# Performance work log

Measured on AMD Instinct MI355X. Metric: run time of the kernel, lower is better.

## Reference

```python
import jax, jax.numpy as jnp
import numpy as np

_EPS = 1e-5

def _ln(x, g, b):
    m = jnp.mean(x, axis=-1, keepdims=True)
    v = jnp.var(x, axis=-1, keepdims=True)
    return (x - m) * jax.lax.rsqrt(v + _EPS) * g + b

def setup_inputs() -> dict:
    key = jax.random.key(0)
    ks = jax.random.split(key, 12)
    B, S, D = 8, 2048, 1024
    H = 2 * D          # hidden_dim = 2*n_embd
    A = H // 16        # adapt_dim = 128
    E = 8              # num_experts
    std = 1.0 / D ** 0.5
    astd = std * 0.01
    f = lambda k, shape, s: jax.random.normal(k, shape, dtype=jnp.float32) * s
    return {
        'x': f(ks[0], (B, S, D), 1.0),
        'expert_weights': f(ks[1], (B, S, E), 1.0),
        'w_up': f(ks[2], (H, D), std),
        'w_gate': f(ks[3], (H, D), std),
        'w_down': f(ks[4], (D, H), std),
        'w_pre': f(ks[5], (A, D), astd),
        'w_post': f(ks[6], (A, H), astd),
        'an_g': jnp.ones((A,), jnp.float32),
        'an_b': jnp.zeros((A,), jnp.float32),
        'w_aproj': f(ks[7], (H, A), astd),
        'w_exp': f(ks[8], (E, A, A), 0.01 / A ** 0.5),
        'eln_g': jnp.ones((E, A), jnp.float32),
        'eln_b': jnp.zeros((E, A), jnp.float32),
        'w_eproj': f(ks[9], (H, A), 0.01 / A ** 0.5),
        'w_out': f(ks[10], (D, H), 0.01 / A ** 0.5),
    }

def reference(x, expert_weights, w_up, w_gate, w_down, w_pre, w_post,
              an_g, an_b, w_aproj, w_exp, eln_g, eln_b, w_eproj, w_out):
    # ---- shared LLaDAExpert ----
    up = jnp.einsum('bsd,hd->bsh', x, w_up)
    gate = jnp.einsum('bsd,hd->bsh', x, w_gate)
    hidden = jax.nn.silu(gate) * up                      # [B,S,H]
    pre = jnp.einsum('bsd,ad->bsa', x, w_pre)            # pre_adapt(x), reused by experts
    adapt_in = _ln(pre, an_g, an_b)                      # [B,S,A]
    adapt_out = _ln(jnp.einsum('bsh,ah->bsa', hidden, w_post), an_g, an_b)
    aw = jax.nn.silu(jnp.clip(jnp.einsum('bsa,bta->bst', adapt_in, adapt_out), -5.0, 5.0))  # [B,S,S]
    adapt = jnp.einsum('bst,bta->bsa', aw, adapt_in)     # [B,S,A]
    hidden = hidden + 0.1 * jnp.einsum('bsa,ha->bsh', adapt, w_aproj)
    shared = jnp.einsum('bsh,dh->bsd', hidden, w_down)   # [B,S,D]
    combined = jnp.zeros_like(shared)
    E = w_exp.shape[0]
    for i in range(E):
        a = _ln(jnp.einsum('bsa,ca->bsc', pre, w_exp[i]), eln_g[i], eln_b[i])
        o = jnp.einsum('bsh,dh->bsd', jnp.einsum('bsc,hc->bsh', a, w_eproj), w_out)
        mask = expert_weights[:, :, i] > 0
        combined = jnp.where(mask[..., None], o, combined)
    return shared + 0.1 * combined
```

## Files before the change

### kernel.cpp

```cpp
#include <hip/hip_runtime.h>

#define TOK 16384
#define DD 1024
#define HH 2048
#define AA 128
#define EE 8
#define SS 2048
#define BB 8

typedef __attribute__((ext_vector_type(8))) short short8;
typedef __attribute__((ext_vector_type(4))) float floatx4;

__device__ __forceinline__ unsigned short f2b(float f) {
  unsigned u = __float_as_uint(f);
  u += 0x7fff + ((u >> 16) & 1);
  return (unsigned short)(u >> 16);
}
__device__ __forceinline__ float b2f(unsigned short h) {
  return __uint_as_float(((unsigned)h) << 16);
}

__device__ __forceinline__ void xcd_swizzle(int& bx, int& by) {
  const int nbx = gridDim.x, nby = gridDim.y;
  if ((nby & 7) == 0) {
    const int L = blockIdx.y * nbx + blockIdx.x;
    const int xcd = L & 7, idx = L >> 3;
    bx = idx % nbx;
    by = (xcd * (nby >> 3)) + idx / nbx;
  } else {
    bx = blockIdx.x; by = blockIdx.y;
  }
}


__device__ __forceinline__ void gload16(const short* g, short* l) {
  __builtin_amdgcn_global_load_lds((__attribute__((address_space(1))) void*)(void*)g,
                                   (__attribute__((address_space(3))) void*)l, 16, 0, 0);
}

__device__ __forceinline__ void stage_half(const short* src, int ld, short* dst, int wave, int h) {
  gload16(src + (long)(2*h)  *64*ld, dst + (2*h)  *4096 + wave*512);
  gload16(src + (long)(2*h+1)*64*ld, dst + (2*h+1)*4096 + wave*512);
}

#define MFMA_Q(M0, N0)                                                                   \
  __builtin_amdgcn_s_setprio(1);                                                         \
  _Pragma("unroll")                                                                      \
  for (int kk = 0; kk < 2; ++kk)                                                         \
    _Pragma("unroll")                                                                    \
    for (int m = 0; m < 4; ++m)                                                          \
      _Pragma("unroll")                                                                  \
      for (int n = 0; n < 2; ++n)                                                        \
        acc[M0+m][N0+n] = __builtin_amdgcn_mfma_f32_16x16x32_bf16(af[M0+m][kk], bf[N0+n][kk], acc[M0+m][N0+n], 0, 0, 0); \
  __builtin_amdgcn_s_setprio(0);

#define PHASE_END                                                                        \
  asm volatile("s_waitcnt lgkmcnt(0)" ::: "memory");                                     \
  __builtin_amdgcn_s_barrier();                                                          \
  asm volatile("" ::: "memory");

__device__ __forceinline__ void ktile8(const char* cA, const char* cB,
                                       short* nAd, short* cBd,
                                       const short* sA1, int lA1,
                                       const short* sB2, int lB2,
                                       bool stA, bool stB, int wave,
                                       int aOff, int bOff, int slot0, int slot1,
                                       floatx4 (*acc)[4])
{
  short8 af[8][2], bf[4][2];
#pragma unroll
  for (int m = 0; m < 4; ++m) {
    af[m][0] = *(const short8*)(cA + aOff + m*2048 + slot0);
    af[m][1] = *(const short8*)(cA + aOff + m*2048 + slot1);
  }
#pragma unroll
  for (int n = 0; n < 2; ++n) {
    bf[n][0] = *(const short8*)(cB + bOff + n*2048 + slot0);
    bf[n][1] = *(const short8*)(cB + bOff + n*2048 + slot1);
  }
  if (stA) stage_half(sA1, lA1, nAd, wave, 0);
  MFMA_Q(0, 0)
  PHASE_END
#pragma unroll
  for (int n = 2; n < 4; ++n) {
    bf[n][0] = *(const short8*)(cB + bOff + n*2048 + slot0);
    bf[n][1] = *(const short8*)(cB + bOff + n*2048 + slot1);
  }
  if (stA) stage_half(sA1, lA1, nAd, wave, 1);
  MFMA_Q(0, 2)
  PHASE_END
#pragma unroll
  for (int m = 4; m < 8; ++m) {
    af[m][0] = *(const short8*)(cA + aOff + m*2048 + slot0);
    af[m][1] = *(const short8*)(cA + aOff + m*2048 + slot1);
  }
  if (stB) stage_half(sB2, lB2, cBd, wave, 0);
  MFMA_Q(4, 0)
  PHASE_END
  if (stB) stage_half(sB2, lB2, cBd, wave, 1);
  MFMA_Q(4, 2)
  asm volatile("s_waitcnt lgkmcnt(0)" ::: "memory");
  if (stB) asm volatile("s_waitcnt vmcnt(4)" ::: "memory");
  else     asm volatile("s_waitcnt vmcnt(0)" ::: "memory");
  __builtin_amdgcn_s_barrier();
  asm volatile("" ::: "memory");
}

template<int EPI, bool SEG2>
__global__ __launch_bounds__(512, 2)
void gemm256(const unsigned short* __restrict__ Ag, int lda,
             const unsigned short* __restrict__ Bg, int ldb,
             void* __restrict__ Cg, int ldc,
             const unsigned short* __restrict__ Xg, int ldx,
             int K1,
             const unsigned short* __restrict__ A2g, int lda2,
             const unsigned short* __restrict__ B2g, int ldb2,
             int K2)
{
  __shared__ __align__(16) short As0[256*64], As1[256*64];
  __shared__ __align__(16) short Bs0[256*64], Bs1[256*64];
  int bx, by; xcd_swizzle(bx, by);
  const int tid = threadIdx.x;
  const int lane = tid & 63, wave = tid >> 6;
  const int q = lane >> 4, l15 = lane & 15;
  const int wm = wave >> 2, wn = wave & 3;

  const int arow = tid >> 3;
  const int kc8  = ((tid & 7) ^ (arow & 7)) * 8;

  const short* a1 = (const short*)Ag + (long)(by*256 + arow)*lda + kc8;
  const short* b1 = (const short*)Bg + (long)(bx*256 + arow)*ldb + kc8;
  const short* a2 = SEG2 ? (const short*)A2g + (long)(by*256 + arow)*lda2 + kc8 : (const short*)0;
  const short* b2 = SEG2 ? (const short*)B2g + (long)(bx*256 + arow)*ldb2 + kc8 : (const short*)0;
  const int nt1 = K1 >> 6, nt = SEG2 ? ((K1 + K2) >> 6) : (K1 >> 6);

  auto tA = [&](int T, const short*& p, int& ld) {
    if (!SEG2 || T < nt1) { p = a1 + T*64; ld = lda; } else { p = a2 + (T - nt1)*64; ld = lda2; }
  };
  auto tB = [&](int T, const short*& p, int& ld) {
    if (!SEG2 || T < nt1) { p = b1 + T*64; ld = ldb; } else { p = b2 + (T - nt1)*64; ld = ldb2; }
  };

  const int aOff  = (wm*128 + l15) * 128;
  const int bOff  = (wn*64  + l15) * 128;
  const int l7    = l15 & 7;
  const int slot0 = ((0*4 + q) ^ l7) * 16;
  const int slot1 = ((1*4 + q) ^ l7) * 16;

  floatx4 acc[8][4] = {};

  stage_half(a1, lda, As0, wave, 0); stage_half(a1, lda, As0, wave, 1);
  stage_half(b1, ldb, Bs0, wave, 0); stage_half(b1, ldb, Bs0, wave, 1);
  {
    const short *pb; int lb;
    tB(1, pb, lb);
    stage_half(pb, lb, Bs1, wave, 0); stage_half(pb, lb, Bs1, wave, 1);
  }
  asm volatile("s_waitcnt vmcnt(4)" ::: "memory");
  __builtin_amdgcn_s_barrier();
  asm volatile("" ::: "memory");

  for (int t = 0; t < nt; t += 2) {
    const short *sa, *sb; int la, lb;
    {
      const bool stA = (t+1) < nt, stB = (t+2) < nt;
      sa = a1; la = lda; sb = b1; lb = ldb;
      if (stA) tA(t+1, sa, la);
      if (stB) tB(t+2, sb, lb);
      ktile8((const char*)As0, (const char*)Bs0, As1, Bs0,
             sa, la, sb, lb, stA, stB, wave, aOff, bOff, slot0, slot1, acc);
    }
    {
      const bool stA = (t+2) < nt, stB = (t+3) < nt;
      sa = a1; la = lda; sb = b1; lb = ldb;
      if (stA) tA(t+2, sa, la);
      if (stB) tB(t+3, sb, lb);
      ktile8((const char*)As1, (const char*)Bs1, As0, Bs1,
             sa, la, sb, lb, stA, stB, wave, aOff, bOff, slot0, slot1, acc);
    }
  }

#pragma unroll
  for (int m = 0; m < 8; ++m)
#pragma unroll
    for (int n = 0; n < 4; ++n)
#pragma unroll
      for (int r = 0; r < 4; ++r) {
        const int row = by*256 + wm*128 + m*16 + q*4 + r;
        const int col = bx*256 + wn*64  + n*16 + l15;
        const long ci = (long)row*ldc + col;
        float v = acc[m][n][r];
        if (EPI == 0) {
          ((float*)Cg)[ci] = v;
        } else if (EPI == 1) {
          v = v / (1.f + __expf(-v));
          ((unsigned short*)Cg)[ci] = f2b(v);
        } else if (EPI == 2) {
          float g = b2f(Xg[(long)row*ldx + col]);
          ((unsigned short*)Cg)[ci] = f2b(v * g);
        }
      }
}

__device__ __forceinline__ void kloop_pipe(const short* Ap, int lda, const short* Bp, int ldb,
                                           short* As, short* Bs, int K,
                                           int tid, int q, int l15, int l7, int wm, int wn,
                                           floatx4 (*acc)[4])
{
  short8 pa[4], pb[4];
#pragma unroll
  for (int i = 0; i < 4; ++i) {
    pa[i] = *(const short8*)(Ap + (long)i*32*lda);
    pb[i] = *(const short8*)(Bp + (long)i*32*ldb);
  }
  for (int kt = 0; kt < K; kt += 64) {
#pragma unroll
    for (int i = 0; i < 4; ++i) {
      *(short8*)((char*)As + i*4096 + tid*16) = pa[i];
      *(short8*)((char*)Bs + i*4096 + tid*16) = pb[i];
    }
    __syncthreads();
    if (kt + 64 < K) {
#pragma unroll
      for (int i = 0; i < 4; ++i) {
        pa[i] = *(const short8*)(Ap + (long)i*32*lda + kt + 64);
        pb[i] = *(const short8*)(Bp + (long)i*32*ldb + kt + 64);
      }
    }
#pragma unroll
    for (int s = 0; s < 2; ++s) {
      short8 af[4], bf[4];
      const int slotoff = ((s*4 + q) ^ l7) * 16;
#pragma unroll
      for (int i = 0; i < 4; ++i) {
        af[i] = *(const short8*)((const char*)As + (wm*64 + i*16 + l15)*128 + slotoff);
        bf[i] = *(const short8*)((const char*)Bs + (wn*64 + i*16 + l15)*128 + slotoff);
      }
#pragma unroll
      for (int i = 0; i < 4; ++i)
#pragma unroll
        for (int j = 0; j < 4; ++j)
          acc[i][j] = __builtin_amdgcn_mfma_f32_16x16x32_bf16(af[i], bf[j], acc[i][j], 0, 0, 0);
    }
    __syncthreads();
  }
}

__global__ void cast_f32_bf16(const float* __restrict__ in, unsigned short* __restrict__ out, long n4) {
  long i = (long)blockIdx.x * blockDim.x + threadIdx.x;
  const long stride = (long)gridDim.x * blockDim.x;
  for (; i < n4; i += stride) {
    float4 v = ((const float4*)in)[i];
    ushort4 o;
    o.x = f2b(v.x); o.y = f2b(v.y); o.z = f2b(v.z); o.w = f2b(v.w);
    ((ushort4*)out)[i] = o;
  }
}

__global__ void transpose_cast(const float* __restrict__ in, unsigned short* __restrict__ out,
                               int R, int C) {
  __shared__ float t[32][33];
  const int lx = threadIdx.x & 31, ly = threadIdx.x >> 5;
  const int r0 = blockIdx.y * 32, c0 = blockIdx.x * 32;
#pragma unroll
  for (int i = 0; i < 32; i += 8)
    t[ly + i][lx] = in[(long)(r0 + ly + i) * C + (c0 + lx)];
  __syncthreads();
#pragma unroll
  for (int i = 0; i < 32; i += 8)
    out[(long)(c0 + ly + i) * R + (r0 + lx)] = f2b(t[lx][ly + i]);
}

template<int EPI>
__global__ __launch_bounds__(256)
void gemm_bt(const unsigned short* __restrict__ Ag, long sAz, int lda,
             const unsigned short* __restrict__ Bg, long sBz, int ldb,
             void* __restrict__ Cg, long sCz, int ldc,
             const unsigned short* __restrict__ Xg, long sXz, int ldx,
             int K)
{
  __shared__ __align__(16) short As[128*64];
  __shared__ __align__(16) short Bs[128*64];
  int bx, by; xcd_swizzle(bx, by);
  const int tid  = threadIdx.x;
  const int lane = tid & 63, wave = tid >> 6;
  const int q = lane >> 4, l15 = lane & 15, l7 = lane & 7;
  const int wm = wave & 1, wn = wave >> 1;

  const int arow = tid >> 3;
  const int kc8  = ((tid & 7) ^ (arow & 7)) * 8;

  const short* Ap = (const short*)Ag + (long)blockIdx.z*sAz + (long)(by*128 + arow)*lda + kc8;
  const short* Bp = (const short*)Bg + (long)blockIdx.z*sBz + (long)(bx*128 + arow)*ldb + kc8;

  floatx4 acc[4][4] = {};
  kloop_pipe(Ap, lda, Bp, ldb, As, Bs, K, tid, q, l15, l7, wm, wn, acc);

  const long cz = (long)blockIdx.z * sCz;
  const long xz = (long)blockIdx.z * sXz;
#pragma unroll
  for (int i = 0; i < 4; ++i)
#pragma unroll
    for (int j = 0; j < 4; ++j)
#pragma unroll
      for (int r = 0; r < 4; ++r) {
        const int row = by*128 + wm*64 + i*16 + q*4 + r;
        const int col = bx*128 + wn*64 + j*16 + l15;
        const long ci = cz + (long)row*ldc + col;
        float v = acc[i][j][r];
        if (EPI == 0) {
          ((float*)Cg)[ci] = v;
        } else if (EPI == 1) {
          v = v / (1.f + __expf(-v));
          ((unsigned short*)Cg)[ci] = f2b(v);
        } else if (EPI == 2) {
          float g = b2f(Xg[xz + (long)row*ldx + col]);
          ((unsigned short*)Cg)[ci] = f2b(v * g);
        } else if (EPI == 3) {
          ((unsigned short*)Cg)[ci] = f2b(v);
        } else if (EPI == 4) {
          v = fminf(fmaxf(v, -5.f), 5.f);
          v = v / (1.f + __expf(-v));
          ((unsigned short*)Cg)[ci] = f2b(v);
        } else if (EPI == 6) {
          ((unsigned short*)Cg)[ci] = f2b(0.1f * v);
        }
      }
}

__global__ void ln_rows(const float* __restrict__ X, const float* __restrict__ X2,
                        const float* __restrict__ g,
                        const float* __restrict__ b, unsigned short* __restrict__ lnout,
                        unsigned short* __restrict__ rawout, unsigned short* __restrict__ tout)
{
  const int lane = threadIdx.x & 63, wave = threadIdx.x >> 6;
  const long t = (long)blockIdx.x*4 + wave;
  const float* x  = X  + t*AA;
  const float* x2 = X2 + t*AA;
  float x0 = x[lane]      + x2[lane];
  float x1 = x[lane + 64] + x2[lane + 64];
  float s = x0 + x1, s2 = x0*x0 + x1*x1;
#pragma unroll
  for (int m = 1; m < 64; m <<= 1) {
    s  += __shfl_xor(s, m, 64);
    s2 += __shfl_xor(s2, m, 64);
  }
  float mean = s * (1.f/AA);
  float inv  = rsqrtf(s2*(1.f/AA) - mean*mean + 1e-5f);
  float y0 = (x0 - mean)*inv*g[lane] + b[lane];
  float y1 = (x1 - mean)*inv*g[lane+64] + b[lane+64];
  lnout[t*AA + lane]      = f2b(y0);
  lnout[t*AA + lane + 64] = f2b(y1);
  if (rawout) { rawout[t*AA+lane] = f2b(x0); rawout[t*AA+lane+64] = f2b(x1); }
  if (tout) {
    const long bb = t >> 11, si = t & (SS-1);
    tout[bb*(long)AA*SS + (long)lane*SS + si]      = f2b(y0);
    tout[bb*(long)AA*SS + (long)(lane+64)*SS + si] = f2b(y1);
  }
}

__global__ void expert_select_ln(const float* __restrict__ ew, const unsigned short* __restrict__ eall,
                                 const float* __restrict__ eg, const float* __restrict__ ebias,
                                 unsigned short* __restrict__ Fc)
{
  const int lane = threadIdx.x & 63, wave = threadIdx.x >> 6;
  const long t = (long)blockIdx.x*4 + wave;
  const float* w = ew + t*EE;
  int ie = -1;
#pragma unroll
  for (int i = 0; i < EE; ++i) if (w[i] > 0.f) ie = i;
  unsigned short o0 = 0, o1 = 0;
  if (ie >= 0) {
    float x0 = b2f(eall[t*(EE*AA) + ie*AA + lane]);
    float x1 = b2f(eall[t*(EE*AA) + ie*AA + lane + 64]);
    float s = x0 + x1, s2 = x0*x0 + x1*x1;
#pragma unroll
    for (int m = 1; m < 64; m <<= 1) { s += __shfl_xor(s, m, 64); s2 += __shfl_xor(s2, m, 64); }
    float mean = s * (1.f/AA);
    float inv  = rsqrtf(s2*(1.f/AA) - mean*mean + 1e-5f);
    o0 = f2b((x0-mean)*inv*eg[ie*AA+lane]    + ebias[ie*AA+lane]);
    o1 = f2b((x1-mean)*inv*eg[ie*AA+lane+64] + ebias[ie*AA+lane+64]);
  }
  Fc[t*256 + lane]      = o0;
  Fc[t*256 + lane + 64] = o1;
}

extern "C" void kernel_launch(void* const* d_in, const int* in_sizes, int n_in,
                              void* d_out, int out_size, void* d_ws, size_t ws_size,
                              hipStream_t stream)
{
  const float* x       = (const float*)d_in[0];
  const float* ew      = (const float*)d_in[1];
  const float* w_up    = (const float*)d_in[2];
  const float* w_gate  = (const float*)d_in[3];
  const float* w_down  = (const float*)d_in[4];
  const float* w_pre   = (const float*)d_in[5];
  const float* w_post  = (const float*)d_in[6];
  const float* an_g    = (const float*)d_in[7];
  const float* an_b    = (const float*)d_in[8];
  const float* w_aproj = (const float*)d_in[9];
  const float* w_exp   = (const float*)d_in[10];
  const float* eln_g   = (const float*)d_in[11];
  const float* eln_b   = (const float*)d_in[12];
  const float* w_eproj = (const float*)d_in[13];
  const float* w_out   = (const float*)d_in[14];

  char* ws = (char*)d_ws;
  size_t off = 0;
  auto take = [&](size_t bytes) { char* p = ws + off; off += (bytes + 255) & ~(size_t)255; return p; };

  unsigned short* Sc    = (unsigned short*)take((size_t)BB*SS*SS*2);
  unsigned short* xb    = Sc;
  unsigned short* eall  = (unsigned short*)((char*)Sc + (size_t)TOK*DD*2);
  unsigned short* hid   = (unsigned short*)take((size_t)TOK*HH*2);
  float*          pre   = (float*)take((size_t)TOK*AA*4*2);
  float*          postA = (float*)take((size_t)TOK*AA*4*2);
  unsigned short* Fc    = (unsigned short*)take((size_t)TOK*256*2);
  unsigned short* ain   = (unsigned short*)take((size_t)TOK*AA*2);
  unsigned short* ainT  = (unsigned short*)take((size_t)TOK*AA*2);
  unsigned short* aout  = (unsigned short*)take((size_t)TOK*AA*2);
  unsigned short* preb  = (unsigned short*)take((size_t)TOK*AA*2);
  unsigned short* wgb   = (unsigned short*)take((size_t)HH*DD*2);
  unsigned short* wub   = (unsigned short*)take((size_t)HH*DD*2);
  unsigned short* wdb   = (unsigned short*)take((size_t)DD*HH*2);
  unsigned short* wpostb= (unsigned short*)take((size_t)AA*HH*2);
  unsigned short* wpreb = (unsigned short*)take((size_t)AA*DD*2);
  unsigned short* wexpb = (unsigned short*)take((size_t)EE*AA*AA*2);
  unsigned short* Wc    = (unsigned short*)take((size_t)DD*256*2);
  (void)ws_size; (void)in_sizes; (void)n_in; (void)out_size;

  unsigned short* woutb  = hid;
  unsigned short* btT    = hid + (size_t)DD*HH;
  unsigned short* eprojT = btT;
  unsigned short* aprojT = btT + (size_t)AA*HH;

  cast_f32_bf16<<<1024, 256, 0, stream>>>(x,      xb,     (long)TOK*DD/4);
  cast_f32_bf16<<<256,  256, 0, stream>>>(w_gate, wgb,    (long)HH*DD/4);
  cast_f32_bf16<<<256,  256, 0, stream>>>(w_up,   wub,    (long)HH*DD/4);
  cast_f32_bf16<<<256,  256, 0, stream>>>(w_down, wdb,    (long)DD*HH/4);
  cast_f32_bf16<<<256,  256, 0, stream>>>(w_out,  woutb,  (long)DD*HH/4);
  cast_f32_bf16<<<64,   256, 0, stream>>>(w_post, wpostb, (long)AA*HH/4);
  cast_f32_bf16<<<32,   256, 0, stream>>>(w_pre,  wpreb,  (long)AA*DD/4);
  cast_f32_bf16<<<32,   256, 0, stream>>>(w_exp,  wexpb,  (long)EE*AA*AA/4);

  transpose_cast<<<dim3(AA/32, HH/32), 256, 0, stream>>>(w_eproj, eprojT, HH, AA);
  transpose_cast<<<dim3(AA/32, HH/32), 256, 0, stream>>>(w_aproj, aprojT, HH, AA);

  gemm_bt<6><<<dim3(1, DD/128, 2), 256, 0, stream>>>(
      woutb, (long)(wdb - woutb), HH,
      eprojT, (long)AA*HH, HH,
      Wc, AA, 256, nullptr, 0, 0, HH);

  gemm256<1, false><<<dim3(HH/256, TOK/256), 512, 0, stream>>>(
      xb, DD, wgb, DD, hid, HH, nullptr, 0, DD, nullptr, 0, nullptr, 0, 0);
  gemm256<2, false><<<dim3(HH/256, TOK/256), 512, 0, stream>>>(
      xb, DD, wub, DD, hid, HH, hid, HH, DD, nullptr, 0, nullptr, 0, 0);

  gemm_bt<0><<<dim3(1, TOK/128, 2), 256, 0, stream>>>(
      xb, DD/2, DD, wpreb, DD/2, DD, pre, (long)TOK*AA, AA, nullptr, 0, 0, DD/2);
  ln_rows<<<TOK/4, 256, 0, stream>>>(pre, pre + (size_t)TOK*AA, an_g, an_b, ain, preb, ainT);

  gemm_bt<3><<<dim3((EE*AA)/128, TOK/128, 1), 256, 0, stream>>>(preb,0,AA, wexpb,0,AA, eall,0,EE*AA, nullptr,0,0, AA);
  expert_select_ln<<<TOK/4, 256, 0, stream>>>(ew, eall, eln_g, eln_b, Fc);

  gemm_bt<0><<<dim3(1, TOK/128, 2), 256, 0, stream>>>(
      hid, HH/2, HH, wpostb, HH/2, HH, postA, (long)TOK*AA, AA, nullptr, 0, 0, HH/2);
  ln_rows<<<TOK/4, 256, 0, stream>>>(postA, postA + (size_t)TOK*AA, an_g, an_b, aout, nullptr, nullptr);

  gemm_bt<4><<<dim3(SS/128, SS/128, BB), 256, 0, stream>>>(ain,(long)SS*AA,AA, aout,(long)SS*AA,AA,
                                                           Sc,(long)SS*SS,SS, nullptr,0,0, AA);
  gemm_bt<3><<<dim3(1, SS/128, BB), 256, 0, stream>>>(Sc,(long)SS*SS,SS, ainT,(long)AA*SS,SS,
                                                      Fc+AA,(long)SS*256,256, nullptr,0,0, SS);
  gemm256<0, true><<<dim3(DD/256, TOK/256), 512, 0, stream>>>(
      hid, HH, wdb, HH, (float*)d_out, DD, nullptr, 0, HH, Fc, 256, Wc, 256, 256);
}
```

Measured before the change: 572.2 us.

## Rebalance gemm256 A/B staging, fuse weight casts, split-K the adapt GEMM

The 256x256 GEMM k-loop now prefetches A tiles further ahead, spreading the A and B half-tile global loads more evenly across the four MFMA phases and raising the allowed in-flight count. The eight separate f32-to-bf16 cast launches become one multi-job kernel to cut launch overhead. The aw·adapt_in GEMM, which had only 128 blocks, is split along K into two halves written to fp32 scratch, then summed and cast into Fc by a small extra kernel. This adds parallelism and removes launches in exchange for extra scratch traffic, an additional kernel, and a risk that pre-buffer reuse or the vmcnt accounting is wrong.

```diff
diff --git a/kernel.cpp b/kernel.cpp
--- a/kernel.cpp
+++ b/kernel.cpp
@@ -60,10 +60,11 @@
   asm volatile("" ::: "memory");
 
 __device__ __forceinline__ void ktile8(const char* cA, const char* cB,
-                                       short* nAd, short* cBd,
+                                       short* oAd, short* cAd, short* cBd,
                                        const short* sA1, int lA1,
+                                       const short* sA2, int lA2,
                                        const short* sB2, int lB2,
-                                       bool stA, bool stB, int wave,
+                                       bool st1, bool st2, int wave,
                                        int aOff, int bOff, int slot0, int slot1,
                                        floatx4 (*acc)[4])
 {
@@ -78,7 +79,7 @@
     bf[n][0] = *(const short8*)(cB + bOff + n*2048 + slot0);
     bf[n][1] = *(const short8*)(cB + bOff + n*2048 + slot1);
   }
-  if (stA) stage_half(sA1, lA1, nAd, wave, 0);
+  if (st1) stage_half(sA1, lA1, oAd, wave, 1);
   MFMA_Q(0, 0)
   PHASE_END
 #pragma unroll
@@ -86,7 +87,6 @@
     bf[n][0] = *(const short8*)(cB + bOff + n*2048 + slot0);
     bf[n][1] = *(const short8*)(cB + bOff + n*2048 + slot1);
   }
-  if (stA) stage_half(sA1, lA1, nAd, wave, 1);
   MFMA_Q(0, 2)
   PHASE_END
 #pragma unroll
@@ -94,13 +94,16 @@
     af[m][0] = *(const short8*)(cA + aOff + m*2048 + slot0);
     af[m][1] = *(const short8*)(cA + aOff + m*2048 + slot1);
   }
-  if (stB) stage_half(sB2, lB2, cBd, wave, 0);
+  if (st2) stage_half(sB2, lB2, cBd, wave, 0);
   MFMA_Q(4, 0)
   PHASE_END
-  if (stB) stage_half(sB2, lB2, cBd, wave, 1);
+  if (st2) {
+    stage_half(sB2, lB2, cBd, wave, 1);
+    stage_half(sA2, lA2, cAd, wave, 0);
+  }
   MFMA_Q(4, 2)
   asm volatile("s_waitcnt lgkmcnt(0)" ::: "memory");
-  if (stB) asm volatile("s_waitcnt vmcnt(4)" ::: "memory");
+  if (st2) asm volatile("s_waitcnt vmcnt(6)" ::: "memory");
   else     asm volatile("s_waitcnt vmcnt(0)" ::: "memory");
   __builtin_amdgcn_s_barrier();
   asm volatile("" ::: "memory");
@@ -152,31 +155,34 @@
   stage_half(a1, lda, As0, wave, 0); stage_half(a1, lda, As0, wave, 1);
   stage_half(b1, ldb, Bs0, wave, 0); stage_half(b1, ldb, Bs0, wave, 1);
   {
-    const short *pb; int lb;
-    tB(1, pb, lb);
+    const short *pb, *pa; int lb, la;
+    tB(1, pb, lb); tA(1, pa, la);
     stage_half(pb, lb, Bs1, wave, 0); stage_half(pb, lb, Bs1, wave, 1);
-  }
-  asm volatile("s_waitcnt vmcnt(4)" ::: "memory");
+    stage_half(pa, la, As1, wave, 0);
+  }
+  asm volatile("s_waitcnt vmcnt(6)" ::: "memory");
   __builtin_amdgcn_s_barrier();
   asm volatile("" ::: "memory");
 
   for (int t = 0; t < nt; t += 2) {
-    const short *sa, *sb; int la, lb;
+    const short *pa1, *pa2, *pb2; int la1, la2, lb2;
     {
-      const bool stA = (t+1) < nt, stB = (t+2) < nt;
-      sa = a1; la = lda; sb = b1; lb = ldb;
-      if (stA) tA(t+1, sa, la);
-      if (stB) tB(t+2, sb, lb);
-      ktile8((const char*)As0, (const char*)Bs0, As1, Bs0,
-             sa, la, sb, lb, stA, stB, wave, aOff, bOff, slot0, slot1, acc);
+      const bool st1 = (t+1) < nt, st2 = (t+2) < nt;
+      pa1 = a1; la1 = lda; pa2 = a1; la2 = lda; pb2 = b1; lb2 = ldb;
+      if (st1) tA(t+1, pa1, la1);
+      if (st2) { tA(t+2, pa2, la2); tB(t+2, pb2, lb2); }
+      ktile8((const char*)As0, (const char*)Bs0, As1, As0, Bs0,
+             pa1, la1, pa2, la2, pb2, lb2, st1, st2, wave,
+             aOff, bOff, slot0, slot1, acc);
     }
     {
-      const bool stA = (t+2) < nt, stB = (t+3) < nt;
-      sa = a1; la = lda; sb = b1; lb = ldb;
-      if (stA) tA(t+2, sa, la);
-      if (stB) tB(t+3, sb, lb);
-      ktile8((const char*)As1, (const char*)Bs1, As0, Bs1,
-             sa, la, sb, lb, stA, stB, wave, aOff, bOff, slot0, slot1, acc);
+      const bool st1 = (t+2) < nt, st2 = (t+3) < nt;
+      pa1 = a1; la1 = lda; pa2 = a1; la2 = lda; pb2 = b1; lb2 = ldb;
+      if (st1) tA(t+2, pa1, la1);
+      if (st2) { tA(t+3, pa2, la2); tB(t+3, pb2, lb2); }
+      ktile8((const char*)As1, (const char*)Bs1, As0, As1, Bs1,
+             pa1, la1, pa2, la2, pb2, lb2, st1, st2, wave,
+             aOff, bOff, slot0, slot1, acc);
     }
   }
 
@@ -246,14 +252,24 @@
   }
 }
 
-__global__ void cast_f32_bf16(const float* __restrict__ in, unsigned short* __restrict__ out, long n4) {
+struct CastJobs {
+  const float* src[8];
+  unsigned short* dst[8];
+  long end[8];
+};
+__global__ void cast_multi(CastJobs jobs, long total4) {
   long i = (long)blockIdx.x * blockDim.x + threadIdx.x;
   const long stride = (long)gridDim.x * blockDim.x;
-  for (; i < n4; i += stride) {
-    float4 v = ((const float4*)in)[i];
-    ushort4 o;
-    o.x = f2b(v.x); o.y = f2b(v.y); o.z = f2b(v.z); o.w = f2b(v.w);
-    ((ushort4*)out)[i] = o;
+  for (; i < total4; i += stride) {
+    int r = 0; long base = 0;
+#pragma unroll
+    for (int k = 0; k < 7; ++k)
+      if (i >= jobs.end[k]) { r = k + 1; base = jobs.end[k]; }
+    const long o = i - base;
+    float4 v = ((const float4*)jobs.src[r])[o];
+    ushort4 u;
+    u.x = f2b(v.x); u.y = f2b(v.y); u.z = f2b(v.z); u.w = f2b(v.w);
+    ((ushort4*)jobs.dst[r])[o] = u;
   }
 }
 
@@ -271,7 +287,7 @@
     out[(long)(c0 + ly + i) * R + (r0 + lx)] = f2b(t[lx][ly + i]);
 }
 
-template<int EPI>
+template<int EPI, bool SK2 = false>
 __global__ __launch_bounds__(256)
 void gemm_bt(const unsigned short* __restrict__ Ag, long sAz, int lda,
              const unsigned short* __restrict__ Bg, long sBz, int ldb,
@@ -290,14 +306,17 @@
   const int arow = tid >> 3;
   const int kc8  = ((tid & 7) ^ (arow & 7)) * 8;
 
-  const short* Ap = (const short*)Ag + (long)blockIdx.z*sAz + (long)(by*128 + arow)*lda + kc8;
-  const short* Bp = (const short*)Bg + (long)blockIdx.z*sBz + (long)(bx*128 + arow)*ldb + kc8;
+  int zb = blockIdx.z, kh = 0;
+  if (SK2) { kh = zb & 1; zb >>= 1; }
+
+  const short* Ap = (const short*)Ag + (long)zb*sAz + (long)kh*K + (long)(by*128 + arow)*lda + kc8;
+  const short* Bp = (const short*)Bg + (long)zb*sBz + (long)kh*K + (long)(bx*128 + arow)*ldb + kc8;
 
   floatx4 acc[4][4] = {};
   kloop_pipe(Ap, lda, Bp, ldb, As, Bs, K, tid, q, l15, l7, wm, wn, acc);
 
-  const long cz = (long)blockIdx.z * sCz;
-  const long xz = (long)blockIdx.z * sXz;
+  const long cz = (long)zb * sCz;
+  const long xz = (long)zb * sXz;
 #pragma unroll
   for (int i = 0; i < 4; ++i)
 #pragma unroll
@@ -309,7 +328,8 @@
         const long ci = cz + (long)row*ldc + col;
         float v = acc[i][j][r];
         if (EPI == 0) {
-          ((float*)Cg)[ci] = v;
+          if (SK2 && kh) ((float*)(void*)Xg)[ci] = v;
+          else           ((float*)Cg)[ci] = v;
         } else if (EPI == 1) {
           v = v / (1.f + __expf(-v));
           ((unsigned short*)Cg)[ci] = f2b(v);
@@ -326,6 +346,22 @@
           ((unsigned short*)Cg)[ci] = f2b(0.1f * v);
         }
       }
+}
+
+__global__ void addcast_adapt(const float* __restrict__ p0, const float* __restrict__ p1,
+                              unsigned short* __restrict__ Fc) {
+  const long total = (long)TOK * (AA/4);
+  long i = (long)blockIdx.x * blockDim.x + threadIdx.x;
+  const long stride = (long)gridDim.x * blockDim.x;
+  for (; i < total; i += stride) {
+    const long t = i >> 5, a4 = i & 31;
+    float4 a = ((const float4*)p0)[i];
+    float4 b = ((const float4*)p1)[i];
+    ushort4 u;
+    u.x = f2b(a.x + b.x); u.y = f2b(a.y + b.y);
+    u.z = f2b(a.z + b.z); u.w = f2b(a.w + b.w);
+    *(ushort4*)(Fc + t*256 + AA + a4*4) = u;
+  }
 }
 
 __global__ void ln_rows(const float* __restrict__ X, const float* __restrict__ X2,
@@ -434,14 +470,16 @@
   unsigned short* eprojT = btT;
   unsigned short* aprojT = btT + (size_t)AA*HH;
 
-  cast_f32_bf16<<<1024, 256, 0, stream>>>(x,      xb,     (long)TOK*DD/4);
-  cast_f32_bf16<<<256,  256, 0, stream>>>(w_gate, wgb,    (long)HH*DD/4);
-  cast_f32_bf16<<<256,  256, 0, stream>>>(w_up,   wub,    (long)HH*DD/4);
-  cast_f32_bf16<<<256,  256, 0, stream>>>(w_down, wdb,    (long)DD*HH/4);
-  cast_f32_bf16<<<256,  256, 0, stream>>>(w_out,  woutb,  (long)DD*HH/4);
-  cast_f32_bf16<<<64,   256, 0, stream>>>(w_post, wpostb, (long)AA*HH/4);
-  cast_f32_bf16<<<32,   256, 0, stream>>>(w_pre,  wpreb,  (long)AA*DD/4);
-  cast_f32_bf16<<<32,   256, 0, stream>>>(w_exp,  wexpb,  (long)EE*AA*AA/4);
+  {
+    CastJobs J;
+    const float* s[8]   = { x, w_gate, w_up, w_down, w_out, w_post, w_pre, w_exp };
+    unsigned short* d[8]= { xb, wgb,   wub,  wdb,    woutb, wpostb, wpreb, wexpb };
+    long n4[8] = { (long)TOK*DD/4, (long)HH*DD/4, (long)HH*DD/4, (long)DD*HH/4,
+                   (long)DD*HH/4, (long)AA*HH/4, (long)AA*DD/4, (long)EE*AA*AA/4 };
+    long acc4 = 0;
+    for (int k = 0; k < 8; ++k) { J.src[k] = s[k]; J.dst[k] = d[k]; acc4 += n4[k]; J.end[k] = acc4; }
+    cast_multi<<<2048, 256, 0, stream>>>(J, acc4);
+  }
 
   transpose_cast<<<dim3(AA/32, HH/32), 256, 0, stream>>>(w_eproj, eprojT, HH, AA);
   transpose_cast<<<dim3(AA/32, HH/32), 256, 0, stream>>>(w_aproj, aprojT, HH, AA);
@@ -469,8 +507,11 @@
 
   gemm_bt<4><<<dim3(SS/128, SS/128, BB), 256, 0, stream>>>(ain,(long)SS*AA,AA, aout,(long)SS*AA,AA,
                                                            Sc,(long)SS*SS,SS, nullptr,0,0, AA);
-  gemm_bt<3><<<dim3(1, SS/128, BB), 256, 0, stream>>>(Sc,(long)SS*SS,SS, ainT,(long)AA*SS,SS,
-                                                      Fc+AA,(long)SS*256,256, nullptr,0,0, SS);
+  gemm_bt<0, true><<<dim3(1, SS/128, BB*2), 256, 0, stream>>>(
+      Sc, (long)SS*SS, SS, ainT, (long)AA*SS, SS,
+      pre, (long)SS*AA, AA, (const unsigned short*)(pre + (size_t)TOK*AA), (long)SS*AA, AA, SS/2);
+  addcast_adapt<<<2048, 256, 0, stream>>>(pre, pre + (size_t)TOK*AA, Fc);
+
   gemm256<0, true><<<dim3(DD/256, TOK/256), 512, 0, stream>>>(
       hid, HH, wdb, HH, (float*)d_out, DD, nullptr, 0, HH, Fc, 256, Wc, 256, 256);
 }
```

Measured after the change: 532.2 us. -7.0%, faster.
